# Optimization experiments

Hardware: AMD Instinct MI355X
Metric: run time of the kernel (lower is better)

## Reference

```python
import jax, jax.numpy as jnp
import numpy as np

N, E, C_IN, C_OUT = 50000, 800000, 64, 64
BN_EPS = 1e-5


def _batchnorm(h, gamma, beta):
    # Training-mode BatchNorm1d: batch statistics over dim 0, biased variance.
    mean = h.mean(axis=0)
    var = h.var(axis=0)  # ddof=0, matches PyTorch normalization stats
    return gamma * (h - mean) * jax.lax.rsqrt(var + BN_EPS) + beta


def setup_inputs() -> dict:
    key = jax.random.key(0)
    ks = jax.random.split(key, 6)
    x = jax.random.normal(ks[0], (N, C_IN), dtype=jnp.float32)
    edge_index = jax.random.randint(ks[1], (2, E), 0, N, dtype=jnp.int32)
    edge_weight = jax.random.uniform(ks[2], (E,), dtype=jnp.float32)
    s1 = 1.0 / np.sqrt(C_IN).astype(np.float32)
    s2 = 1.0 / np.sqrt(2 * C_IN).astype(np.float32)
    pool_W = jax.random.uniform(ks[3], (C_IN, C_IN), jnp.float32, -s1, s1)
    pool_b = jnp.zeros((C_IN,), jnp.float32)
    final_W = jax.random.uniform(ks[4], (2 * C_IN, C_OUT), jnp.float32, -s2, s2)
    final_b = jnp.zeros((C_OUT,), jnp.float32)
    return {
        "x": x,
        "edge_index": edge_index,
        "edge_weight": edge_weight,
        "pool_W": pool_W,
        "pool_b": pool_b,
        "bn_pool_gamma": jnp.ones((C_IN,), jnp.float32),
        "bn_pool_beta": jnp.zeros((C_IN,), jnp.float32),
        "final_W": final_W,
        "final_b": final_b,
        "bn_final_gamma": jnp.ones((C_OUT,), jnp.float32),
        "bn_final_beta": jnp.zeros((C_OUT,), jnp.float32),
        "coef": jnp.float32(0.5),
    }


def reference(x, edge_index, edge_weight, pool_W, pool_b, bn_pool_gamma,
              bn_pool_beta, final_W, final_b, bn_final_gamma, bn_final_beta,
              coef):
    src, dst = edge_index[0], edge_index[1]
    # gather src node features, scale by edge weight  -> [E, C_IN]
    edge_feat = x[src] * (1.0 + coef * edge_weight[:, None])
    pooled = edge_feat @ pool_W + pool_b              # [E, C_IN]
    pooled = jax.nn.relu(_batchnorm(pooled, bn_pool_gamma, bn_pool_beta))
    # scatter-max into destination nodes; empty segments -> 0 (pooled >= 0)
    agg = jax.ops.segment_max(pooled, dst, num_segments=x.shape[0])
    agg = jnp.maximum(agg, 0.0)                       # fill -inf (empty) with 0
    h = jnp.concatenate([x, agg], axis=-1) @ final_W + final_b  # [N, C_OUT]
    h = _batchnorm(h, bn_final_gamma, bn_final_beta)
    return jax.nn.relu(h)
```

## Files before the change

kernel.cpp:

```cpp
#include <hip/hip_runtime.h>
#include <hip/hip_fp16.h>
#include <math.h>
#include <float.h>

#define BN_EPS 1e-5f
#define SLOTS 64
#define SB 256


typedef __attribute__((ext_vector_type(8))) short bf16x8;
typedef __attribute__((ext_vector_type(4))) float f32x4;

__device__ inline unsigned short f2bf(float f) {
    unsigned u = __float_as_uint(f);
    return (unsigned short)((u + 0x7fffu + ((u >> 16) & 1u)) >> 16);
}
__device__ inline float bf2f(unsigned short h) {
    return __uint_as_float(((unsigned)h) << 16);
}

__global__ __launch_bounds__(256, 4) void k_scatter_gemm(
        const int* __restrict__ src, const int* __restrict__ dst,
        const float* __restrict__ w, const float* __restrict__ coef_p,
        int* __restrict__ cnt, unsigned* __restrict__ csr, int E,
        const float* __restrict__ x, const float* __restrict__ W,
        unsigned short* __restrict__ ybf, int nrows, int gemmGrid) {
    __shared__ unsigned short Wt[64 * 72];
    if (blockIdx.x < SB) {
        const float coef = *coef_p;
        const int tid = blockIdx.x * 256 + threadIdx.x;
        const int stride4 = SB * 256 * 4;
        for (int base = tid * 4; base < E; base += stride4) {
            if (base + 3 < E) {
                int4   s4 = *(const int4*)(src + base);
                int4   d4 = *(const int4*)(dst + base);
                float4 w4 = *(const float4*)(w + base);
                int sn[4] = {s4.x, s4.y, s4.z, s4.w};
                int dn[4] = {d4.x, d4.y, d4.z, d4.w};
                float wv[4] = {w4.x, w4.y, w4.z, w4.w};
                unsigned hs[4];
                int pos[4];
#pragma unroll
                for (int j = 0; j < 4; ++j) {
                    float s = fmaf(coef, wv[j], 1.0f);
                    hs[j] = (unsigned)__half_as_ushort(__float2half(s));
                    pos[j] = atomicAdd(&cnt[dn[j]], 1);
                }
#pragma unroll
                for (int j = 0; j < 4; ++j)
                    if (pos[j] < SLOTS)
                        csr[(size_t)dn[j] * SLOTS + pos[j]] =
                            ((unsigned)sn[j] << 16) | hs[j];
            } else {
                for (int i = base; i < E; ++i) {
                    int sn = src[i], tn = dst[i];
                    float s = fmaf(coef, w[i], 1.0f);
                    unsigned hs = (unsigned)__half_as_ushort(__float2half(s));
                    int pos = atomicAdd(&cnt[tn], 1);
                    if (pos < SLOTS)
                        csr[(size_t)tn * SLOTS + pos] = ((unsigned)sn << 16) | hs;
                }
            }
        }
        return;
    }
    const int bid = blockIdx.x - SB;
    for (int i = threadIdx.x; i < 64 * 64; i += 256) {
        int k = i >> 6, n = i & 63;
        Wt[n * 72 + k] = f2bf(W[i]);
    }
    __syncthreads();
    const int lane = threadIdx.x & 63;
    const int wave = threadIdx.x >> 6;
    const int quad = lane >> 4;
    const int ln = lane & 15;
    bf16x8 Bf[2][4];
#pragma unroll
    for (int kc = 0; kc < 2; ++kc)
#pragma unroll
        for (int ct = 0; ct < 4; ++ct)
            Bf[kc][ct] = *(const bf16x8*)&Wt[(ct * 16 + ln) * 72 + kc * 32 + quad * 8];
    const int T = (nrows + 15) >> 4;
    const int gw = bid * 4 + wave;
    const int nw = gemmGrid * 4;
    for (int t = gw; t < T; t += nw) {
        const int row = t * 16 + ln;
        bf16x8 af[2];
        if (row < nrows) {
            const float* xr = x + (size_t)row * 64;
#pragma unroll
            for (int kc = 0; kc < 2; ++kc) {
                float4 p = *(const float4*)(xr + kc * 32 + quad * 8);
                float4 q = *(const float4*)(xr + kc * 32 + quad * 8 + 4);
                bf16x8 a;
                a[0] = (short)f2bf(p.x); a[1] = (short)f2bf(p.y);
                a[2] = (short)f2bf(p.z); a[3] = (short)f2bf(p.w);
                a[4] = (short)f2bf(q.x); a[5] = (short)f2bf(q.y);
                a[6] = (short)f2bf(q.z); a[7] = (short)f2bf(q.w);
                af[kc] = a;
            }
        } else {
            bf16x8 z;
#pragma unroll
            for (int j = 0; j < 8; ++j) z[j] = 0;
            af[0] = z; af[1] = z;
        }
        f32x4 acc[4];
#pragma unroll
        for (int ct = 0; ct < 4; ++ct) { acc[ct][0]=0.f; acc[ct][1]=0.f; acc[ct][2]=0.f; acc[ct][3]=0.f; }
#pragma unroll
        for (int ct = 0; ct < 4; ++ct) {
            acc[ct] = __builtin_amdgcn_mfma_f32_16x16x32_bf16(af[0], Bf[0][ct], acc[ct], 0, 0, 0);
            acc[ct] = __builtin_amdgcn_mfma_f32_16x16x32_bf16(af[1], Bf[1][ct], acc[ct], 0, 0, 0);
        }
#pragma unroll
        for (int r = 0; r < 4; ++r) {
            int ro = t * 16 + quad * 4 + r;
            if (ro < nrows) {
#pragma unroll
                for (int ct = 0; ct < 4; ++ct)
                    ybf[(size_t)ro * 64 + ct * 16 + ln] = f2bf(acc[ct][r]);
            }
        }
    }
}

__global__ __launch_bounds__(256) void k_gather_max(const unsigned short* __restrict__ ybf,
                             const unsigned* __restrict__ csr, const int* __restrict__ cnt,
                             float* __restrict__ M, float* __restrict__ partials, int nrows) {
    int t = blockIdx.x * blockDim.x + threadIdx.x;
    int node = t >> 4;
    int sub = threadIdx.x & 15;
    int rg = threadIdx.x >> 4;
    int c0 = sub * 4;
    size_t base = (size_t)node * SLOTS;
    int dg = 0;
    if (node < nrows) { dg = cnt[node]; if (dg > SLOTS) dg = SLOTS; }
    float m0 = -FLT_MAX, m1 = -FLT_MAX, m2 = -FLT_MAX, m3 = -FLT_MAX;
    float s1[4] = {0, 0, 0, 0}, s2[4] = {0, 0, 0, 0};
    for (int k0 = 0; k0 < dg; k0 += 16) {
        int kk = k0 + sub;
        unsigned pk = (kk < dg) ? csr[base + kk] : 0u;
        int rem = dg - k0;
        ushort4 uv[16];
        float sv[16];
#pragma unroll
        for (int j = 0; j < 16; ++j) {
            unsigned r = (unsigned)__shfl((int)pk, j, 16);
            sv[j] = __half2float(__ushort_as_half((unsigned short)(r & 0xffffu)));
            uv[j] = *(const ushort4*)&ybf[(size_t)(r >> 16) * 64 + c0];
        }
#pragma unroll
        for (int j = 0; j < 16; ++j) {
            if (j < rem) {
                float v0 = sv[j] * bf2f(uv[j].x), v1 = sv[j] * bf2f(uv[j].y);
                float v2 = sv[j] * bf2f(uv[j].z), v3 = sv[j] * bf2f(uv[j].w);
                m0 = fmaxf(m0, v0); s1[0] += v0; s2[0] = fmaf(v0, v0, s2[0]);
                m1 = fmaxf(m1, v1); s1[1] += v1; s2[1] = fmaf(v1, v1, s2[1]);
                m2 = fmaxf(m2, v2); s1[2] += v2; s2[2] = fmaf(v2, v2, s2[2]);
                m3 = fmaxf(m3, v3); s1[3] += v3; s2[3] = fmaf(v3, v3, s2[3]);
            }
        }
    }
    if (node < nrows)
        *(float4*)&M[(size_t)node * 64 + c0] = make_float4(m0, m1, m2, m3);
    __shared__ float red[16][68];
#pragma unroll
    for (int j = 0; j < 4; ++j) red[rg][c0 + j] = s1[j];
    __syncthreads();
    if (rg == 0) {
#pragma unroll
        for (int j = 0; j < 4; ++j) {
            float tt = 0.0f;
            for (int r = 0; r < 16; ++r) tt += red[r][c0 + j];
            partials[(size_t)blockIdx.x * 128 + c0 + j] = tt;
        }
    }
    __syncthreads();
#pragma unroll
    for (int j = 0; j < 4; ++j) red[rg][c0 + j] = s2[j];
    __syncthreads();
    if (rg == 0) {
#pragma unroll
        for (int j = 0; j < 4; ++j) {
            float tt = 0.0f;
            for (int r = 0; r < 16; ++r) tt += red[r][c0 + j];
            partials[(size_t)blockIdx.x * 128 + 64 + c0 + j] = tt;
        }
    }
}

__global__ __launch_bounds__(256) void k_red1(const float* __restrict__ partials, int P,
                                              float* __restrict__ p2) {
    int c = threadIdx.x & 127;
    int half = threadIdx.x >> 7;
    float acc = 0.0f;
    for (int r = blockIdx.x * 2 + half; r < P; r += 256)
        acc += partials[(size_t)r * 128 + c];
    __shared__ float sh[256];
    sh[threadIdx.x] = acc;
    __syncthreads();
    if (half == 0) p2[(size_t)blockIdx.x * 128 + c] = sh[c] + sh[128 + c];
}

__global__ __launch_bounds__(1024) void k_red2(const float* __restrict__ p2,
                             const float* __restrict__ pool_b, const float* __restrict__ gamma,
                             const float* __restrict__ beta, float invE,
                             float* __restrict__ coef) {
    int c = threadIdx.x & 127;
    int seg = threadIdx.x >> 7;
    float acc = 0.0f;
    for (int r = seg; r < 128; r += 8) acc += p2[(size_t)r * 128 + c];
    __shared__ float red[8][128];
    red[seg][c] = acc;
    __syncthreads();
    if (seg == 0) {
        float tt = 0.0f;
#pragma unroll
        for (int s = 0; s < 8; ++s) tt += red[s][c];
        red[0][c] = tt;
    }
    __syncthreads();
    if (threadIdx.x < 64) {
        int c0 = threadIdx.x;
        float S1 = red[0][c0], S2 = red[0][64 + c0];
        float s1 = S1 * invE;
        float b = pool_b[c0];
        float mean = s1 + b;
        float ex2 = S2 * invE + 2.0f * b * s1 + b * b;
        float var = ex2 - mean * mean;
        float a = gamma[c0] * rsqrtf(var + BN_EPS);
        coef[c0] = a;
        coef[64 + c0] = beta[c0] - a * s1;
    }
}

__global__ __launch_bounds__(1024) void k_red2f(const float* __restrict__ p2,
                             const float* __restrict__ gamma, const float* __restrict__ beta,
                             float invN, float* __restrict__ coef) {
    int c = threadIdx.x & 127;
    int seg = threadIdx.x >> 7;
    float acc = 0.0f;
    for (int r = seg; r < 128; r += 8) acc += p2[(size_t)r * 128 + c];
    __shared__ float red[8][128];
    red[seg][c] = acc;
    __syncthreads();
    if (seg == 0) {
        float tt = 0.0f;
#pragma unroll
        for (int s = 0; s < 8; ++s) tt += red[s][c];
        red[0][c] = tt;
    }
    __syncthreads();
    if (threadIdx.x < 64) {
        int c0 = threadIdx.x;
        float mean = red[0][c0] * invN;
        float var = red[0][64 + c0] * invN - mean * mean;
        float a = gamma[c0] * rsqrtf(var + BN_EPS);
        coef[c0] = a;
        coef[64 + c0] = beta[c0] - a * mean;
    }
}

__global__ __launch_bounds__(256, 2) void k_final_gemm(const float* __restrict__ x,
                             const float* __restrict__ M, const float* __restrict__ coef,
                             const float* __restrict__ W, const float* __restrict__ b,
                             float* __restrict__ h, float* __restrict__ partials, int nrows) {
    __shared__ unsigned short Wt[64 * 136];
    __shared__ float hp[128];
    for (int i = threadIdx.x; i < 128 * 64; i += 256) {
        int k = i >> 6, n = i & 63;
        Wt[n * 136 + k] = f2bf(W[i]);
    }
    if (threadIdx.x < 128) hp[threadIdx.x] = 0.0f;
    __syncthreads();
    const int lane = threadIdx.x & 63;
    const int wave = threadIdx.x >> 6;
    const int quad = lane >> 4;
    const int ln = lane & 15;
    bf16x8 Bf[4][4];
#pragma unroll
    for (int kc = 0; kc < 4; ++kc)
#pragma unroll
        for (int ct = 0; ct < 4; ++ct)
            Bf[kc][ct] = *(const bf16x8*)&Wt[(ct * 16 + ln) * 136 + kc * 32 + quad * 8];
    float bias[4];
#pragma unroll
    for (int ct = 0; ct < 4; ++ct) bias[ct] = b[ct * 16 + ln];
    float ca[2][8], cd[2][8];
#pragma unroll
    for (int g = 0; g < 2; ++g) {
        int ch = g * 32 + quad * 8;
#pragma unroll
        for (int j = 0; j < 8; ++j) {
            ca[g][j] = coef[ch + j];
            cd[g][j] = coef[64 + ch + j];
        }
    }
    float ls1[4] = {0, 0, 0, 0}, ls2[4] = {0, 0, 0, 0};
    const int T = (nrows + 15) >> 4;
    const int gw = blockIdx.x * 4 + wave;
    const int nw = gridDim.x * 4;
    for (int t = gw; t < T; t += nw) {
        const int row = t * 16 + ln;
        bf16x8 af[4];
        if (row < nrows) {
            const float* xr = x + (size_t)row * 64;
#pragma unroll
            for (int kc = 0; kc < 2; ++kc) {
                float4 p = *(const float4*)(xr + kc * 32 + quad * 8);
                float4 q = *(const float4*)(xr + kc * 32 + quad * 8 + 4);
                bf16x8 a;
                a[0] = (short)f2bf(p.x); a[1] = (short)f2bf(p.y);
                a[2] = (short)f2bf(p.z); a[3] = (short)f2bf(p.w);
                a[4] = (short)f2bf(q.x); a[5] = (short)f2bf(q.y);
                a[6] = (short)f2bf(q.z); a[7] = (short)f2bf(q.w);
                af[kc] = a;
            }
            const float* mr = M + (size_t)row * 64;
#pragma unroll
            for (int g = 0; g < 2; ++g) {
                const float* mp = mr + g * 32 + quad * 8;
                float4 p = *(const float4*)mp;
                float4 q = *(const float4*)(mp + 4);
                float v[8] = {p.x, p.y, p.z, p.w, q.x, q.y, q.z, q.w};
                bf16x8 a;
#pragma unroll
                for (int j = 0; j < 8; ++j)
                    a[j] = (short)f2bf(fmaxf(fmaf(ca[g][j], v[j], cd[g][j]), 0.0f));
                af[2 + g] = a;
            }
        } else {
            bf16x8 z;
#pragma unroll
            for (int j = 0; j < 8; ++j) z[j] = 0;
#pragma unroll
            for (int kc = 0; kc < 4; ++kc) af[kc] = z;
        }
        f32x4 acc[4];
#pragma unroll
        for (int ct = 0; ct < 4; ++ct) { acc[ct][0]=0.f; acc[ct][1]=0.f; acc[ct][2]=0.f; acc[ct][3]=0.f; }
#pragma unroll
        for (int kc = 0; kc < 4; ++kc)
#pragma unroll
            for (int ct = 0; ct < 4; ++ct)
                acc[ct] = __builtin_amdgcn_mfma_f32_16x16x32_bf16(af[kc], Bf[kc][ct], acc[ct], 0, 0, 0);
#pragma unroll
        for (int r = 0; r < 4; ++r) {
            int ro = t * 16 + quad * 4 + r;
            if (ro < nrows) {
#pragma unroll
                for (int ct = 0; ct < 4; ++ct) {
                    float hv = acc[ct][r] + bias[ct];
                    h[(size_t)ro * 64 + ct * 16 + ln] = hv;
                    ls1[ct] += hv;
                    ls2[ct] = fmaf(hv, hv, ls2[ct]);
                }
            }
        }
    }
#pragma unroll
    for (int ct = 0; ct < 4; ++ct) {
        atomicAdd(&hp[ct * 16 + ln], ls1[ct]);
        atomicAdd(&hp[64 + ct * 16 + ln], ls2[ct]);
    }
    __syncthreads();
    if (threadIdx.x < 128)
        partials[(size_t)blockIdx.x * 128 + threadIdx.x] = hp[threadIdx.x];
}

__global__ __launch_bounds__(256) void k_bn_out(const float* __restrict__ h,
                         const float* __restrict__ coef,
                         float* __restrict__ out, int nrows) {
    const int idx = blockIdx.x * blockDim.x + threadIdx.x;
    const int total = nrows * 16;
    if (idx >= total) return;
    const int c0 = (idx & 15) * 4;
    const float4 hv = *(const float4*)(h + (size_t)idx * 4);
    float4 o;
    float* op = (float*)&o;
    const float* hp = (const float*)&hv;
#pragma unroll
    for (int j = 0; j < 4; ++j) {
        const int c = c0 + j;
        op[j] = fmaxf(fmaf(coef[c], hp[j], coef[64 + c]), 0.0f);
    }
    *(float4*)(out + (size_t)idx * 4) = o;
}

extern "C" void kernel_launch(void* const* d_in, const int* in_sizes, int n_in,
                              void* d_out, int out_size, void* d_ws, size_t ws_size,
                              hipStream_t stream) {
    const float* x       = (const float*)d_in[0];
    const int*   eidx    = (const int*)d_in[1];
    const float* ew      = (const float*)d_in[2];
    const float* pool_W  = (const float*)d_in[3];
    const float* pool_b  = (const float*)d_in[4];
    const float* g1      = (const float*)d_in[5];
    const float* b1      = (const float*)d_in[6];
    const float* final_W = (const float*)d_in[7];
    const float* final_b = (const float*)d_in[8];
    const float* g2      = (const float*)d_in[9];
    const float* b2      = (const float*)d_in[10];
    const float* coef    = (const float*)d_in[11];

    const int N = in_sizes[0] / 64;
    const int E = in_sizes[1] / 2;
    const int* src = eidx;
    const int* dst = eidx + E;

    const int PG  = (N * 16 + 255) / 256;
    const int T   = (N + 15) / 16;
    const int nbT = (T + 3) / 4;

    unsigned* ws = (unsigned*)d_ws;
    int*   cnt      = (int*)ws;
    float* bncoef   = (float*)(ws + (size_t)N);
    float* coef2    = (float*)(ws + (size_t)N + 128);
    float* p2       = (float*)(ws + (size_t)N + 256);
    float* p2F      = p2 + 16384;
    float* partialsG= p2F + 16384;
    float* partialsF= partialsG + (size_t)PG * 128;
    unsigned short* ybf = (unsigned short*)(partialsF + (size_t)nbT * 128);
    unsigned* csrF  = (unsigned*)ybf + (size_t)32 * N;
    float* M        = (float*)(csrF + (size_t)SLOTS * N);

    hipMemsetAsync(cnt, 0, (size_t)N * 4, stream);

    k_scatter_gemm<<<SB + nbT, 256, 0, stream>>>(src, dst, ew, coef, cnt, csrF, E,
                                                 x, pool_W, ybf, N, nbT);
    k_gather_max<<<PG, 256, 0, stream>>>(ybf, csrF, cnt, M, partialsG, N);
    k_red1   <<<128, 256, 0, stream>>>(partialsG, PG, p2);
    k_red2   <<<1, 1024, 0, stream>>>(p2, pool_b, g1, b1, 1.0f / (float)E, bncoef);
    k_final_gemm<<<nbT, 256, 0, stream>>>(x, M, bncoef, final_W, final_b,
                                          (float*)d_out, partialsF, N);
    k_red1   <<<128, 256, 0, stream>>>(partialsF, nbT, p2F);
    k_red2f  <<<1, 1024, 0, stream>>>(p2F, g2, b2, 1.0f / (float)N, coef2);
    k_bn_out <<<(N * 16 + 255) / 256, 256, 0, stream>>>((const float*)d_out, coef2,
                                                        (float*)d_out, N);
}
```

Baseline: 201.5 us.

## Precompute x half of final GEMM in scatter kernel; fuse two-stage reductions

Splits the final GEMM: the x·W_top + bias part is computed in the scatter/pool-GEMM kernel by extra blocks and written to an fp32 buffer hx. The final GEMM then only multiplies the normalized agg half and adds hx. It also merges the two reduction kernels in each BN stage into one, using a last-block-done atomic counter. The aim is to take work off the critical path and save two launches, at the cost of an extra N×64 fp32 write and read for hx.

```diff
diff --git a/kernel.cpp b/kernel.cpp
--- a/kernel.cpp
+++ b/kernel.cpp
@@ -23,8 +23,10 @@
         const int* __restrict__ src, const int* __restrict__ dst,
         const float* __restrict__ w, const float* __restrict__ coef_p,
         int* __restrict__ cnt, unsigned* __restrict__ csr, int E,
-        const float* __restrict__ x, const float* __restrict__ W,
-        unsigned short* __restrict__ ybf, int nrows, int gemmGrid) {
+        const float* __restrict__ x, const float* __restrict__ Wp,
+        unsigned short* __restrict__ ybf,
+        const float* __restrict__ Wf, const float* __restrict__ fb,
+        float* __restrict__ hx, int nrows, int g1) {
     __shared__ unsigned short Wt[64 * 72];
     if (blockIdx.x < SB) {
         const float coef = *coef_p;
@@ -64,10 +66,13 @@
         }
         return;
     }
-    const int bid = blockIdx.x - SB;
+    const int gb = blockIdx.x - SB;
+    const int hp_ = (gb >= g1) ? 1 : 0;
+    const int bid = hp_ ? gb - g1 : gb;
+    const float* Wsrc = hp_ ? Wf : Wp;
     for (int i = threadIdx.x; i < 64 * 64; i += 256) {
         int k = i >> 6, n = i & 63;
-        Wt[n * 72 + k] = f2bf(W[i]);
+        Wt[n * 72 + k] = f2bf(Wsrc[i]);
     }
     __syncthreads();
     const int lane = threadIdx.x & 63;
@@ -80,9 +85,12 @@
 #pragma unroll
         for (int ct = 0; ct < 4; ++ct)
             Bf[kc][ct] = *(const bf16x8*)&Wt[(ct * 16 + ln) * 72 + kc * 32 + quad * 8];
+    float bias[4];
+#pragma unroll
+    for (int ct = 0; ct < 4; ++ct) bias[ct] = hp_ ? fb[ct * 16 + ln] : 0.0f;
     const int T = (nrows + 15) >> 4;
     const int gw = bid * 4 + wave;
-    const int nw = gemmGrid * 4;
+    const int nw = g1 * 4;
     for (int t = gw; t < T; t += nw) {
         const int row = t * 16 + ln;
         bf16x8 af[2];
@@ -117,9 +125,15 @@
         for (int r = 0; r < 4; ++r) {
             int ro = t * 16 + quad * 4 + r;
             if (ro < nrows) {
-#pragma unroll
-                for (int ct = 0; ct < 4; ++ct)
-                    ybf[(size_t)ro * 64 + ct * 16 + ln] = f2bf(acc[ct][r]);
+                if (hp_) {
+#pragma unroll
+                    for (int ct = 0; ct < 4; ++ct)
+                        hx[(size_t)ro * 64 + ct * 16 + ln] = acc[ct][r] + bias[ct];
+                } else {
+#pragma unroll
+                    for (int ct = 0; ct < 4; ++ct)
+                        ybf[(size_t)ro * 64 + ct * 16 + ln] = f2bf(acc[ct][r]);
+                }
             }
         }
     }
@@ -190,8 +204,11 @@
     }
 }
 
-__global__ __launch_bounds__(256) void k_red1(const float* __restrict__ partials, int P,
-                                              float* __restrict__ p2) {
+__global__ __launch_bounds__(256) void k_redG(const float* __restrict__ partials, int P,
+                             float* __restrict__ p2, int* __restrict__ done,
+                             const float* __restrict__ pool_b, const float* __restrict__ gamma,
+                             const float* __restrict__ beta, float invE,
+                             float* __restrict__ coef) {
     int c = threadIdx.x & 127;
     int half = threadIdx.x >> 7;
     float acc = 0.0f;
@@ -201,29 +218,22 @@
     sh[threadIdx.x] = acc;
     __syncthreads();
     if (half == 0) p2[(size_t)blockIdx.x * 128 + c] = sh[c] + sh[128 + c];
-}
-
-__global__ __launch_bounds__(1024) void k_red2(const float* __restrict__ p2,
-                             const float* __restrict__ pool_b, const float* __restrict__ gamma,
-                             const float* __restrict__ beta, float invE,
-                             float* __restrict__ coef) {
-    int c = threadIdx.x & 127;
-    int seg = threadIdx.x >> 7;
-    float acc = 0.0f;
-    for (int r = seg; r < 128; r += 8) acc += p2[(size_t)r * 128 + c];
-    __shared__ float red[8][128];
-    red[seg][c] = acc;
-    __syncthreads();
-    if (seg == 0) {
-        float tt = 0.0f;
-#pragma unroll
-        for (int s = 0; s < 8; ++s) tt += red[s][c];
-        red[0][c] = tt;
-    }
+    __threadfence();
+    __syncthreads();
+    __shared__ int lastf;
+    if (threadIdx.x == 0) lastf = (atomicAdd(done, 1) == (int)gridDim.x - 1);
+    __syncthreads();
+    if (!lastf) return;
+    __threadfence();
+    float a2 = 0.0f;
+    for (int r = half; r < 128; r += 2) a2 += p2[(size_t)r * 128 + c];
+    __shared__ float s2r[2][128];
+    s2r[half][c] = a2;
     __syncthreads();
     if (threadIdx.x < 64) {
         int c0 = threadIdx.x;
-        float S1 = red[0][c0], S2 = red[0][64 + c0];
+        float S1 = s2r[0][c0] + s2r[1][c0];
+        float S2 = s2r[0][64 + c0] + s2r[1][64 + c0];
         float s1 = S1 * invE;
         float b = pool_b[c0];
         float mean = s1 + b;
@@ -235,42 +245,52 @@
     }
 }
 
-__global__ __launch_bounds__(1024) void k_red2f(const float* __restrict__ p2,
+__global__ __launch_bounds__(256) void k_redF(const float* __restrict__ partials, int P,
+                             float* __restrict__ p2, int* __restrict__ done,
                              const float* __restrict__ gamma, const float* __restrict__ beta,
                              float invN, float* __restrict__ coef) {
     int c = threadIdx.x & 127;
-    int seg = threadIdx.x >> 7;
+    int half = threadIdx.x >> 7;
     float acc = 0.0f;
-    for (int r = seg; r < 128; r += 8) acc += p2[(size_t)r * 128 + c];
-    __shared__ float red[8][128];
-    red[seg][c] = acc;
-    __syncthreads();
-    if (seg == 0) {
-        float tt = 0.0f;
-#pragma unroll
-        for (int s = 0; s < 8; ++s) tt += red[s][c];
-        red[0][c] = tt;
-    }
+    for (int r = blockIdx.x * 2 + half; r < P; r += 256)
+        acc += partials[(size_t)r * 128 + c];
+    __shared__ float sh[256];
+    sh[threadIdx.x] = acc;
+    __syncthreads();
+    if (half == 0) p2[(size_t)blockIdx.x * 128 + c] = sh[c] + sh[128 + c];
+    __threadfence();
+    __syncthreads();
+    __shared__ int lastf;
+    if (threadIdx.x == 0) lastf = (atomicAdd(done, 1) == (int)gridDim.x - 1);
+    __syncthreads();
+    if (!lastf) return;
+    __threadfence();
+    float a2 = 0.0f;
+    for (int r = half; r < 128; r += 2) a2 += p2[(size_t)r * 128 + c];
+    __shared__ float s2r[2][128];
+    s2r[half][c] = a2;
     __syncthreads();
     if (threadIdx.x < 64) {
         int c0 = threadIdx.x;
-        float mean = red[0][c0] * invN;
-        float var = red[0][64 + c0] * invN - mean * mean;
+        float S1 = s2r[0][c0] + s2r[1][c0];
+        float S2 = s2r[0][64 + c0] + s2r[1][64 + c0];
+        float mean = S1 * invN;
+        float var = S2 * invN - mean * mean;
         float a = gamma[c0] * rsqrtf(var + BN_EPS);
         coef[c0] = a;
         coef[64 + c0] = beta[c0] - a * mean;
     }
 }
 
-__global__ __launch_bounds__(256, 2) void k_final_gemm(const float* __restrict__ x,
+__global__ __launch_bounds__(256, 4) void k_final_gemm(const float* __restrict__ hx,
                              const float* __restrict__ M, const float* __restrict__ coef,
-                             const float* __restrict__ W, const float* __restrict__ b,
+                             const float* __restrict__ Wb,
                              float* __restrict__ h, float* __restrict__ partials, int nrows) {
-    __shared__ unsigned short Wt[64 * 136];
+    __shared__ unsigned short Wt[64 * 72];
     __shared__ float hp[128];
-    for (int i = threadIdx.x; i < 128 * 64; i += 256) {
+    for (int i = threadIdx.x; i < 64 * 64; i += 256) {
         int k = i >> 6, n = i & 63;
-        Wt[n * 136 + k] = f2bf(W[i]);
+        Wt[n * 72 + k] = f2bf(Wb[i]);
     }
     if (threadIdx.x < 128) hp[threadIdx.x] = 0.0f;
     __syncthreads();
@@ -278,15 +298,12 @@
     const int wave = threadIdx.x >> 6;
     const int quad = lane >> 4;
     const int ln = lane & 15;
-    bf16x8 Bf[4][4];
-#pragma unroll
-    for (int kc = 0; kc < 4; ++kc)
+    bf16x8 Bf[2][4];
+#pragma unroll
+    for (int kc = 0; kc < 2; ++kc)
 #pragma unroll
         for (int ct = 0; ct < 4; ++ct)
-            Bf[kc][ct] = *(const bf16x8*)&Wt[(ct * 16 + ln) * 136 + kc * 32 + quad * 8];
-    float bias[4];
-#pragma unroll
-    for (int ct = 0; ct < 4; ++ct) bias[ct] = b[ct * 16 + ln];
+            Bf[kc][ct] = *(const bf16x8*)&Wt[(ct * 16 + ln) * 72 + kc * 32 + quad * 8];
     float ca[2][8], cd[2][8];
 #pragma unroll
     for (int g = 0; g < 2; ++g) {
@@ -303,20 +320,8 @@
     const int nw = gridDim.x * 4;
     for (int t = gw; t < T; t += nw) {
         const int row = t * 16 + ln;
-        bf16x8 af[4];
+        bf16x8 af[2];
         if (row < nrows) {
-            const float* xr = x + (size_t)row * 64;
-#pragma unroll
-            for (int kc = 0; kc < 2; ++kc) {
-                float4 p = *(const float4*)(xr + kc * 32 + quad * 8);
-                float4 q = *(const float4*)(xr + kc * 32 + quad * 8 + 4);
-                bf16x8 a;
-                a[0] = (short)f2bf(p.x); a[1] = (short)f2bf(p.y);
-                a[2] = (short)f2bf(p.z); a[3] = (short)f2bf(p.w);
-                a[4] = (short)f2bf(q.x); a[5] = (short)f2bf(q.y);
-                a[6] = (short)f2bf(q.z); a[7] = (short)f2bf(q.w);
-                af[kc] = a;
-            }
             const float* mr = M + (size_t)row * 64;
 #pragma unroll
             for (int g = 0; g < 2; ++g) {
@@ -328,20 +333,19 @@
 #pragma unroll
                 for (int j = 0; j < 8; ++j)
                     a[j] = (short)f2bf(fmaxf(fmaf(ca[g][j], v[j], cd[g][j]), 0.0f));
-                af[2 + g] = a;
+                af[g] = a;
             }
         } else {
             bf16x8 z;
 #pragma unroll
             for (int j = 0; j < 8; ++j) z[j] = 0;
-#pragma unroll
-            for (int kc = 0; kc < 4; ++kc) af[kc] = z;
+            af[0] = z; af[1] = z;
         }
         f32x4 acc[4];
 #pragma unroll
         for (int ct = 0; ct < 4; ++ct) { acc[ct][0]=0.f; acc[ct][1]=0.f; acc[ct][2]=0.f; acc[ct][3]=0.f; }
 #pragma unroll
-        for (int kc = 0; kc < 4; ++kc)
+        for (int kc = 0; kc < 2; ++kc)
 #pragma unroll
             for (int ct = 0; ct < 4; ++ct)
                 acc[ct] = __builtin_amdgcn_mfma_f32_16x16x32_bf16(af[kc], Bf[kc][ct], acc[ct], 0, 0, 0);
@@ -351,7 +355,7 @@
             if (ro < nrows) {
 #pragma unroll
                 for (int ct = 0; ct < 4; ++ct) {
-                    float hv = acc[ct][r] + bias[ct];
+                    float hv = acc[ct][r] + hx[(size_t)ro * 64 + ct * 16 + ln];
                     h[(size_t)ro * 64 + ct * 16 + ln] = hv;
                     ls1[ct] += hv;
                     ls2[ct] = fmaf(hv, hv, ls2[ct]);
@@ -415,27 +419,30 @@
 
     unsigned* ws = (unsigned*)d_ws;
     int*   cnt      = (int*)ws;
-    float* bncoef   = (float*)(ws + (size_t)N);
-    float* coef2    = (float*)(ws + (size_t)N + 128);
-    float* p2       = (float*)(ws + (size_t)N + 256);
+    int*   done     = (int*)(ws + (size_t)N);
+    float* bncoef   = (float*)(ws + (size_t)N + 64);
+    float* coef2    = bncoef + 128;
+    float* p2       = coef2 + 128;
     float* p2F      = p2 + 16384;
     float* partialsG= p2F + 16384;
     float* partialsF= partialsG + (size_t)PG * 128;
     unsigned short* ybf = (unsigned short*)(partialsF + (size_t)nbT * 128);
     unsigned* csrF  = (unsigned*)ybf + (size_t)32 * N;
     float* M        = (float*)(csrF + (size_t)SLOTS * N);
-
-    hipMemsetAsync(cnt, 0, (size_t)N * 4, stream);
-
-    k_scatter_gemm<<<SB + nbT, 256, 0, stream>>>(src, dst, ew, coef, cnt, csrF, E,
-                                                 x, pool_W, ybf, N, nbT);
+    float* hx       = M + (size_t)64 * N;
+
+    hipMemsetAsync(cnt, 0, ((size_t)N + 64) * 4, stream);
+
+    k_scatter_gemm<<<SB + 2 * nbT, 256, 0, stream>>>(src, dst, ew, coef, cnt, csrF, E,
+                                                     x, pool_W, ybf,
+                                                     final_W, final_b, hx, N, nbT);
     k_gather_max<<<PG, 256, 0, stream>>>(ybf, csrF, cnt, M, partialsG, N);
-    k_red1   <<<128, 256, 0, stream>>>(partialsG, PG, p2);
-    k_red2   <<<1, 1024, 0, stream>>>(p2, pool_b, g1, b1, 1.0f / (float)E, bncoef);
-    k_final_gemm<<<nbT, 256, 0, stream>>>(x, M, bncoef, final_W, final_b,
+    k_redG<<<128, 256, 0, stream>>>(partialsG, PG, p2, &done[0],
+                                    pool_b, g1, b1, 1.0f / (float)E, bncoef);
+    k_final_gemm<<<nbT, 256, 0, stream>>>(hx, M, bncoef, final_W + 64 * 64,
                                           (float*)d_out, partialsF, N);
-    k_red1   <<<128, 256, 0, stream>>>(partialsF, nbT, p2F);
-    k_red2f  <<<1, 1024, 0, stream>>>(p2F, g2, b2, 1.0f / (float)N, coef2);
-    k_bn_out <<<(N * 16 + 255) / 256, 256, 0, stream>>>((const float*)d_out, coef2,
-                                                        (float*)d_out, N);
-}
+    k_redF<<<128, 256, 0, stream>>>(partialsF, nbT, p2F, &done[1],
+                                    g2, b2, 1.0f / (float)N, coef2);
+    k_bn_out<<<(N * 16 + 255) / 256, 256, 0, stream>>>((const float*)d_out, coef2,
+                                                       (float*)d_out, N);
+}
```

Result: slower. 237.0 us (+17.7%).
